# Kernel optimization log

Measured on AMD Instinct MI355X. Metric: run time of the kernel, lower is better.

## Reference

```python
import jax, jax.numpy as jnp
import numpy as np

WS = 7       # window_size
SHIFT = 3    # shift_size
HEADS = 3
EPS = 1e-5


def _rel_index():
    # (2, N) coords of a WS x WS window, then pairwise relative offsets -> flat table index
    coords = np.stack(np.meshgrid(np.arange(WS), np.arange(WS), indexing='ij')).reshape(2, -1)
    rel = (coords[:, :, None] - coords[:, None, :]).transpose(1, 2, 0) + (WS - 1)  # (N,N,2)
    return jnp.asarray(rel[..., 0] * (2 * WS - 1) + rel[..., 1])  # (N,N) int


def _layernorm(x, g, b):
    mu = jnp.mean(x, axis=-1, keepdims=True)
    var = jnp.mean(jnp.square(x - mu), axis=-1, keepdims=True)
    return (x - mu) * jax.lax.rsqrt(var + EPS) * g + b


def setup_inputs() -> dict:
    key = jax.random.key(0)
    ks = jax.random.split(key, 6)
    C, HID = 96, 384
    s = 0.02
    return {
        'x': jax.random.normal(ks[0], (8, C, 224, 224), jnp.float32),
        'norm1_g': jnp.ones((C,), jnp.float32),
        'norm1_b': jnp.zeros((C,), jnp.float32),
        'qkv_w': jax.random.normal(ks[1], (C, 3 * C), jnp.float32) * s,
        'qkv_b': jnp.zeros((3 * C,), jnp.float32),
        'proj_w': jax.random.normal(ks[2], (C, C), jnp.float32) * s,
        'proj_b': jnp.zeros((C,), jnp.float32),
        'rel_bias_table': jax.random.normal(ks[3], ((2 * WS - 1) ** 2, HEADS), jnp.float32) * s,
        'norm2_g': jnp.ones((C,), jnp.float32),
        'norm2_b': jnp.zeros((C,), jnp.float32),
        'fc1_w': jax.random.normal(ks[4], (C, HID), jnp.float32) * s,
        'fc1_b': jnp.zeros((HID,), jnp.float32),
        'fc2_w': jax.random.normal(ks[5], (HID, C), jnp.float32) * s,
        'fc2_b': jnp.zeros((C,), jnp.float32),
    }


def reference(x, norm1_g, norm1_b, qkv_w, qkv_b, proj_w, proj_b,
              rel_bias_table, norm2_g, norm2_b, fc1_w, fc1_b, fc2_w, fc2_b):
    B, C, H, W = x.shape
    N = WS * WS
    dh = C // HEADS

    # norm1 over channels (tokens = flattened spatial)
    xt = x.reshape(B, C, H * W).transpose(0, 2, 1)          # (B, L, C)
    xn = _layernorm(xt, norm1_g, norm1_b)
    xs = xn.transpose(0, 2, 1).reshape(B, C, H, W)
    # H, W divisible by WS -> pad is a no-op; cyclic shift
    xs = jnp.roll(xs, (-SHIFT, -SHIFT), axis=(2, 3))

    # window partition -> (B*nW, N, C)
    xw = xs.reshape(B, C, H // WS, WS, W // WS, WS)
    xw = xw.transpose(0, 2, 4, 3, 5, 1).reshape(-1, N, C)

    # window attention with relative position bias (no shift mask, per source)
    Bw = xw.shape[0]
    qkv = (xw @ qkv_w + qkv_b).reshape(Bw, N, 3, HEADS, dh).transpose(2, 0, 3, 1, 4)
    q, k, v = qkv[0], qkv[1], qkv[2]                        # (Bw, h, N, dh)
    attn = jnp.einsum('bhnd,bhmd->bhnm', q, k) * (dh ** -0.5)
    bias = rel_bias_table[_rel_index().reshape(-1)].reshape(N, N, HEADS).transpose(2, 0, 1)
    attn = jax.nn.softmax(attn + bias, axis=-1)
    out = jnp.einsum('bhnm,bhmd->bhnd', attn, v).transpose(0, 2, 1, 3).reshape(Bw, N, C)
    out = out @ proj_w + proj_b

    # window reverse + unshift
    xr = out.reshape(B, H // WS, W // WS, WS, WS, C)
    xr = xr.transpose(0, 5, 1, 3, 2, 4).reshape(B, C, H, W)
    xr = jnp.roll(xr, (SHIFT, SHIFT), axis=(2, 3))

    x = x + xr                                              # residual 1

    # MLP branch with norm2 (exact GELU, matching torch nn.GELU default)
    xt = x.reshape(B, C, H * W).transpose(0, 2, 1)
    xn = _layernorm(xt, norm2_g, norm2_b)
    h = jax.nn.gelu(xn @ fc1_w + fc1_b, approximate=False)
    h = h @ fc2_w + fc2_b
    return x + h.transpose(0, 2, 1).reshape(B, C, H, W)
```

## Files before the change

### kernel.cpp

```cpp
#include <hip/hip_runtime.h>
#include <hip/hip_bf16.h>
#include <math.h>

#define WSZ 7
#define NTOK 49
#define CH 96
#define HIMG 224
#define WIMG 224
#define HWIMG (224*224)
#define SHIFT_ 3
#define HID 384

typedef __attribute__((ext_vector_type(8))) short bf16x8;
typedef __attribute__((ext_vector_type(4))) float f32x4;
typedef unsigned int u32;
typedef unsigned short u16;

__device__ __forceinline__ u32 pk2(float a, float b) {
    u16 ua = __builtin_bit_cast(u16, __float2bfloat16(a));
    u16 ub = __builtin_bit_cast(u16, __float2bfloat16(b));
    return (u32)ua | ((u32)ub << 16);
}
__device__ __forceinline__ float bflo(u32 u) { return __builtin_bit_cast(float, u << 16); }

union FragU { u32 w[4]; bf16x8 v; };

__device__ __forceinline__ bf16x8 regroup(u32 t0w0, u32 t0w1, u32 t1w0, u32 t1w1, int lane) {
    int sl0 = (lane & 15) + ((lane & 16) << 1);
    int sl1 = sl0 + 16;
    u32 x0 = (u32)__shfl((int)t0w0, sl0);
    u32 y0 = (u32)__shfl((int)t1w0, sl0);
    u32 x1 = (u32)__shfl((int)t0w1, sl0);
    u32 y1 = (u32)__shfl((int)t1w1, sl0);
    u32 x2 = (u32)__shfl((int)t0w0, sl1);
    u32 y2 = (u32)__shfl((int)t1w0, sl1);
    u32 x3 = (u32)__shfl((int)t0w1, sl1);
    u32 y3 = (u32)__shfl((int)t1w1, sl1);
    bool lo = lane < 32;
    FragU f;
    f.w[0] = lo ? x0 : y0;
    f.w[1] = lo ? x1 : y1;
    f.w[2] = lo ? x2 : y2;
    f.w[3] = lo ? x3 : y3;
    return f.v;
}

__device__ __forceinline__ float gelu_f(float x) {
    float x2 = x * x;
    float s  = x * (0.7978845608028654f + 0.03567740813636141f * x2);
    float e  = __expf(2.0f * s);
    float th = 1.0f - 2.0f / (e + 1.0f);
    return 0.5f * x * (1.0f + th);
}

__global__ __launch_bounds__(256) void prep_kernel(
    const float* __restrict__ w1, const float* __restrict__ w2,
    const float* __restrict__ pw, const float* __restrict__ qw,
    __hip_bfloat16* __restrict__ ws, int n)
{
    int i = blockIdx.x * 256 + threadIdx.x;
    if (i >= n) return;
    float val = 0.f;
    if (i < 81920) {
        int ch = i / 20480, r = i - ch * 20480;
        int half = r / 10240;
        int rr = r - half * 10240;
        if (rr < 9984) {
            int row = rr / 104, col = rr - row * 104;
            if (col < 96)
                val = (half == 0) ? w1[col * HID + ch * 96 + row]
                                  : w2[(size_t)(ch * 96 + col) * CH + row];
        }
    } else if (i < 92160) {
        int r = i - 81920;
        if (r < 9984) {
            int row = r / 104, col = r - row * 104;
            if (col < 96) val = pw[col * CH + row];
        }
    } else {
        int j = i - 92160;
        int hh = j / 9984, rr = j - hh * 9984;
        int dp = rr / 104, c = rr - dp * 104;
        if (c < 96) {
            int colW = (dp < 32) ? (hh * 32 + dp)
                     : (dp < 64) ? (96 + hh * 32 + dp - 32)
                                 : (192 + hh * 32 + dp - 64);
            val = qw[c * 288 + colW];
        }
    }
    ws[i] = __float2bfloat16(val);
}

__global__ __launch_bounds__(256) void attn2_kernel(
    const float* __restrict__ x,
    const float* __restrict__ g1, const float* __restrict__ b1,
    const __hip_bfloat16* __restrict__ wsW,
    const float* __restrict__ qkv_b, const float* __restrict__ pb,
    const float* __restrict__ btab,
    __hip_bfloat16* __restrict__ projout)
{
    const int tid  = threadIdx.x;
    const int lane = tid & 63;
    const int wv   = tid >> 6;
    const int l15  = lane & 15;
    const int g    = lane >> 4;
    const int bi   = blockIdx.x;
    const int b    = bi >> 8;
    const int wh   = (bi >> 3) & 31;
    const int ww0  = (bi & 7) * 4;
    const int ww   = ww0 + wv;

    __shared__ float btabL[507];
    __shared__ __align__(16) char uniA[43008];

    __hip_bfloat16 (*xsb)[7][32] = (__hip_bfloat16(*)[7][32])uniA;
    __hip_bfloat16 (*vT)[72] = (__hip_bfloat16(*)[72])(uniA + wv * 4608);
    u32* prS = (u32*)(uniA + wv * 4608);

    for (int idx = tid; idx < 507; idx += 256) btabL[idx] = btab[idx];

    const int colBase = ww0 * 7 + 3;
    const int cA  = colBase & ~3;
    const int cb4 = cA >> 2;
    const int a0  = colBase & 3;
    #pragma unroll
    for (int k = 0; k < 21; ++k) {
        int idx = tid + 256 * k;
        int c = idx / 56, rem = idx - c * 56;
        int r = rem >> 3, cf = rem & 7;
        int gr = wh * 7 + 3 + r; if (gr >= HIMG) gr -= HIMG;
        int g4 = cb4 + cf; if (g4 >= 56) g4 -= 56;
        float4 v = *(const float4*)(x + ((size_t)(b * CH + c) * HIMG + gr) * WIMG + g4 * 4);
        uint2 pk;
        pk.x = pk2(v.x, v.y);
        pk.y = pk2(v.z, v.w);
        *(uint2*)&xsb[c][r][cf * 4] = pk;
    }
    __syncthreads();

    bf16x8 xB[4][3];
    #pragma unroll
    for (int it = 0; it < 4; ++it) {
        int i = it * 16 + l15;
        bool real = i < NTOK;
        int yi = i / 7, xi = i - yi * 7;
        int sc = a0 + wv * 7 + xi;
        float raw[24];
        float s0 = 0.f, s1 = 0.f;
        #pragma unroll
        for (int ks = 0; ks < 3; ++ks)
            #pragma unroll
            for (int t = 0; t < 8; ++t) {
                int c = ks * 32 + g * 8 + t;
                float v = real ? __bfloat162float(xsb[c][yi][sc]) : 0.f;
                raw[ks * 8 + t] = v; s0 += v; s1 += v * v;
            }
        s0 += __shfl_xor(s0, 16); s0 += __shfl_xor(s0, 32);
        s1 += __shfl_xor(s1, 16); s1 += __shfl_xor(s1, 32);
        float mu = s0 * (1.0f / CH);
        float rstd = rsqrtf(s1 * (1.0f / CH) - mu * mu + 1e-5f);
        #pragma unroll
        for (int ks = 0; ks < 3; ++ks)
            #pragma unroll
            for (int t = 0; t < 8; ++t) {
                int c = ks * 32 + g * 8 + t;
                float xv = real ? ((raw[ks * 8 + t] - mu) * rstd * g1[c] + b1[c]) : 0.f;
                xB[it][ks][t] = (short)__builtin_bit_cast(u16, __float2bfloat16(xv));
            }
    }
    __syncthreads();

    const float scale = 0.17677669529663687f;
    bf16x8 aoB[3][4];

    for (int h = 0; h < 3; ++h) {
        const __hip_bfloat16* qkvTg = wsW + 92160 + h * 9984;

        float qb[2][4], kb[2][4], vb[2][4];
        #pragma unroll
        for (int dt = 0; dt < 2; ++dt)
            #pragma unroll
            for (int r = 0; r < 4; ++r) {
                int d = h * 32 + dt * 16 + g * 4 + r;
                qb[dt][r] = qkv_b[d];
                kb[dt][r] = qkv_b[96 + d];
                vb[dt][r] = qkv_b[192 + d];
            }

        u32 Qpk[2][4][2];
        #pragma unroll
        for (int dt = 0; dt < 2; ++dt) {
            const __hip_bfloat16* wr = qkvTg + (dt * 16 + l15) * 104 + g * 8;
            bf16x8 a0f = *(const bf16x8*)(wr);
            bf16x8 a1f = *(const bf16x8*)(wr + 32);
            bf16x8 a2f = *(const bf16x8*)(wr + 64);
            #pragma unroll
            for (int it = 0; it < 4; ++it) {
                f32x4 c4 = {0.f, 0.f, 0.f, 0.f};
                c4 = __builtin_amdgcn_mfma_f32_16x16x32_bf16(a0f, xB[it][0], c4, 0, 0, 0);
                c4 = __builtin_amdgcn_mfma_f32_16x16x32_bf16(a1f, xB[it][1], c4, 0, 0, 0);
                c4 = __builtin_amdgcn_mfma_f32_16x16x32_bf16(a2f, xB[it][2], c4, 0, 0, 0);
                Qpk[dt][it][0] = pk2(c4[0] + qb[dt][0], c4[1] + qb[dt][1]);
                Qpk[dt][it][1] = pk2(c4[2] + qb[dt][2], c4[3] + qb[dt][3]);
            }
        }
        bf16x8 QB[4];
        #pragma unroll
        for (int it = 0; it < 4; ++it)
            QB[it] = regroup(Qpk[0][it][0], Qpk[0][it][1], Qpk[1][it][0], Qpk[1][it][1], lane);

        u32 Kpk[2][4][2];
        #pragma unroll
        for (int dt = 0; dt < 2; ++dt) {
            const __hip_bfloat16* wr = qkvTg + (32 + dt * 16 + l15) * 104 + g * 8;
            bf16x8 a0f = *(const bf16x8*)(wr);
            bf16x8 a1f = *(const bf16x8*)(wr + 32);
            bf16x8 a2f = *(const bf16x8*)(wr + 64);
            #pragma unroll
            for (int it = 0; it < 4; ++it) {
                f32x4 c4 = {0.f, 0.f, 0.f, 0.f};
                c4 = __builtin_amdgcn_mfma_f32_16x16x32_bf16(a0f, xB[it][0], c4, 0, 0, 0);
                c4 = __builtin_amdgcn_mfma_f32_16x16x32_bf16(a1f, xB[it][1], c4, 0, 0, 0);
                c4 = __builtin_amdgcn_mfma_f32_16x16x32_bf16(a2f, xB[it][2], c4, 0, 0, 0);
                Kpk[dt][it][0] = pk2(c4[0] + kb[dt][0], c4[1] + kb[dt][1]);
                Kpk[dt][it][1] = pk2(c4[2] + kb[dt][2], c4[3] + kb[dt][3]);
            }
        }
        bf16x8 KA[4];
        #pragma unroll
        for (int it = 0; it < 4; ++it)
            KA[it] = regroup(Kpk[0][it][0], Kpk[0][it][1], Kpk[1][it][0], Kpk[1][it][1], lane);

        #pragma unroll
        for (int dt = 0; dt < 2; ++dt) {
            const __hip_bfloat16* wr = qkvTg + (64 + dt * 16 + l15) * 104 + g * 8;
            bf16x8 a0f = *(const bf16x8*)(wr);
            bf16x8 a1f = *(const bf16x8*)(wr + 32);
            bf16x8 a2f = *(const bf16x8*)(wr + 64);
            #pragma unroll
            for (int it = 0; it < 4; ++it) {
                f32x4 c4 = {0.f, 0.f, 0.f, 0.f};
                c4 = __builtin_amdgcn_mfma_f32_16x16x32_bf16(a0f, xB[it][0], c4, 0, 0, 0);
                c4 = __builtin_amdgcn_mfma_f32_16x16x32_bf16(a1f, xB[it][1], c4, 0, 0, 0);
                c4 = __builtin_amdgcn_mfma_f32_16x16x32_bf16(a2f, xB[it][2], c4, 0, 0, 0);
                #pragma unroll
                for (int r = 0; r < 4; ++r)
                    vT[dt * 16 + g * 4 + r][it * 16 + l15] = __float2bfloat16(c4[r] + vb[dt][r]);
            }
        }
        bf16x8 VBf[2][2];
        #pragma unroll
        for (int dt = 0; dt < 2; ++dt)
            #pragma unroll
            for (int ks = 0; ks < 2; ++ks)
                VBf[dt][ks] = *(const bf16x8*)&vT[dt * 16 + l15][ks * 32 + g * 8];

        #pragma unroll
        for (int it = 0; it < 4; ++it) {
            f32x4 SC[4];
            #pragma unroll
            for (int jt = 0; jt < 4; ++jt) {
                f32x4 z = {0.f, 0.f, 0.f, 0.f};
                SC[jt] = __builtin_amdgcn_mfma_f32_16x16x32_bf16(KA[jt], QB[it], z, 0, 0, 0);
            }
            int i = it * 16 + l15;
            int yi = i / 7, xi = i - yi * 7;
            float p[16];
            float m = -1e30f;
            #pragma unroll
            for (int jt = 0; jt < 4; ++jt)
                #pragma unroll
                for (int r = 0; r < 4; ++r) {
                    int j = jt * 16 + g * 4 + r;
                    int yj = j / 7, xj = j - yj * 7;
                    int rel = (yi - yj + 6) * 13 + (xi - xj + 6);
                    rel = rel < 0 ? 0 : (rel > 168 ? 168 : rel);
                    float s = (j < NTOK) ? (SC[jt][r] * scale + btabL[rel * 3 + h]) : -1e30f;
                    p[jt * 4 + r] = s;
                    m = fmaxf(m, s);
                }
            m = fmaxf(m, __shfl_xor(m, 16));
            m = fmaxf(m, __shfl_xor(m, 32));
            float sum = 0.f;
            #pragma unroll
            for (int q = 0; q < 16; ++q) { float e = __expf(p[q] - m); p[q] = e; sum += e; }
            sum += __shfl_xor(sum, 16);
            sum += __shfl_xor(sum, 32);
            float inv = 1.f / sum;
            u32 Ppk[4][2];
            #pragma unroll
            for (int jt = 0; jt < 4; ++jt) {
                Ppk[jt][0] = pk2(p[jt * 4 + 0] * inv, p[jt * 4 + 1] * inv);
                Ppk[jt][1] = pk2(p[jt * 4 + 2] * inv, p[jt * 4 + 3] * inv);
            }
            bf16x8 PA0 = regroup(Ppk[0][0], Ppk[0][1], Ppk[1][0], Ppk[1][1], lane);
            bf16x8 PA1 = regroup(Ppk[2][0], Ppk[2][1], Ppk[3][0], Ppk[3][1], lane);
            u32 opk[2][2];
            #pragma unroll
            for (int dt = 0; dt < 2; ++dt) {
                f32x4 o = {0.f, 0.f, 0.f, 0.f};
                o = __builtin_amdgcn_mfma_f32_16x16x32_bf16(PA0, VBf[dt][0], o, 0, 0, 0);
                o = __builtin_amdgcn_mfma_f32_16x16x32_bf16(PA1, VBf[dt][1], o, 0, 0, 0);
                opk[dt][0] = pk2(o[0], o[1]);
                opk[dt][1] = pk2(o[2], o[3]);
            }
            aoB[h][it] = regroup(opk[0][0], opk[0][1], opk[1][0], opk[1][1], lane);
        }
    }

    const __hip_bfloat16* pwTg = wsW + 81920;
    for (int it = 0; it < 4; ++it) {
        #pragma unroll
        for (int mt = 0; mt < 6; ++mt) {
            const __hip_bfloat16* wr = pwTg + (mt * 16 + l15) * 104 + g * 8;
            f32x4 cp = {0.f, 0.f, 0.f, 0.f};
            #pragma unroll
            for (int ks = 0; ks < 3; ++ks) {
                bf16x8 af = *(const bf16x8*)(wr + ks * 32);
                cp = __builtin_amdgcn_mfma_f32_16x16x32_bf16(af, aoB[ks][it], cp, 0, 0, 0);
            }
            float v0 = cp[0] + pb[mt * 16 + g * 4 + 0];
            float v1 = cp[1] + pb[mt * 16 + g * 4 + 1];
            float v2 = cp[2] + pb[mt * 16 + g * 4 + 2];
            float v3 = cp[3] + pb[mt * 16 + g * 4 + 3];
            prS[l15 * 52 + mt * 8 + g * 2 + 0] = pk2(v0, v1);
            prS[l15 * 52 + mt * 8 + g * 2 + 1] = pk2(v2, v3);
        }
        #pragma unroll
        for (int s = 0; s < 3; ++s) {
            int chunk = lane + 64 * s;
            int row = chunk / 12, q = chunk - row * 12;
            int tok = it * 16 + row;
            if (tok < NTOK) {
                int yi = tok / 7, xi = tok - yi * 7;
                int hh = wh * 7 + yi + SHIFT_; if (hh >= HIMG) hh -= HIMG;
                int wp = ww * 7 + xi + SHIFT_; if (wp >= WIMG) wp -= WIMG;
                float4 val = *(const float4*)((const char*)prS + row * 208 + q * 16);
                *(float4*)(projout + ((size_t)b * HWIMG + hh * WIMG + wp) * 96 + q * 8) = val;
            }
        }
    }
}

__global__ __launch_bounds__(512, 4) void mlp2_kernel(
    const float* __restrict__ x, const __hip_bfloat16* __restrict__ projout,
    const float* __restrict__ g2, const float* __restrict__ b2,
    const float* __restrict__ bb1, const float* __restrict__ bb2,
    const __hip_bfloat16* __restrict__ wsW,
    float* __restrict__ out)
{
    const int tid = threadIdx.x;
    const int lane = tid & 63, wv = tid >> 6;
    const int l15 = lane & 15, g = lane >> 4;
    const int b = blockIdx.x / 392;
    const int hw0 = (blockIdx.x % 392) * 128;
    const int tok = wv * 16 + l15;

    __shared__ __align__(16) char SB[26624];
    __shared__ float bb1S[HID];

    __hip_bfloat16 (*xnS)[104]  = (__hip_bfloat16(*)[104])SB;
    __hip_bfloat16 (*wT)[104]   = (__hip_bfloat16(*)[104])SB;
    __hip_bfloat16 (*obuf)[104] = (__hip_bfloat16(*)[104])SB;

    #pragma unroll
    for (int s = 0; s < 3; ++s) {
        int chunk = tid + 512 * s;
        int row = chunk / 12, q = chunk - row * 12;
        *(float4*)&xnS[row][q * 8] =
            *(const float4*)(projout + ((size_t)b * HWIMG + hw0 + row) * 96 + q * 8);
    }
    for (int idx = tid; idx < HID; idx += 512) bb1S[idx] = bb1[idx];
    __syncthreads();

    float xr[24];
    float s0 = 0.f, s1 = 0.f;
    bf16x8 pf[3];
    #pragma unroll
    for (int ks = 0; ks < 3; ++ks)
        pf[ks] = *(const bf16x8*)&xnS[tok][ks * 32 + g * 8];
    const float* xb = x + (size_t)(b * CH) * HWIMG + hw0 + tok;
    #pragma unroll
    for (int ks = 0; ks < 3; ++ks)
        #pragma unroll
        for (int j = 0; j < 8; ++j) {
            int c = ks * 32 + g * 8 + j;
            float xv = xb[(size_t)c * HWIMG];
            float v = xv + bflo((u32)(u16)pf[ks][j]);
            xr[ks * 8 + j] = v; s0 += v; s1 += v * v;
        }
    s0 += __shfl_xor(s0, 16); s0 += __shfl_xor(s0, 32);
    s1 += __shfl_xor(s1, 16); s1 += __shfl_xor(s1, 32);
    float mu = s0 * (1.0f / CH);
    float rstd = rsqrtf(s1 * (1.0f / CH) - mu * mu + 1e-5f);

    bf16x8 xbf[3];
    #pragma unroll
    for (int ks = 0; ks < 3; ++ks) {
        float nv[8];
        #pragma unroll
        for (int j = 0; j < 8; ++j) {
            int c = ks * 32 + g * 8 + j;
            nv[j] = (xr[ks * 8 + j] - mu) * rstd * g2[c] + b2[c];
        }
        FragU f;
        f.w[0] = pk2(nv[0], nv[1]); f.w[1] = pk2(nv[2], nv[3]);
        f.w[2] = pk2(nv[4], nv[5]); f.w[3] = pk2(nv[6], nv[7]);
        xbf[ks] = f.v;
    }
    __syncthreads();

    f32x4 acc[6];
    #pragma unroll
    for (int mt = 0; mt < 6; ++mt) {
        #pragma unroll
        for (int r = 0; r < 4; ++r) acc[mt][r] = bb2[mt * 16 + g * 4 + r];
    }

    for (int ch = 0; ch < 4; ++ch) {
        {
            const float4* src = (const float4*)wsW + (size_t)ch * 2560;
            #pragma unroll
            for (int i = tid; i < 1280; i += 512) ((float4*)SB)[i] = src[i];
        }
        __syncthreads();

        u32 hpk[6][2];
        #pragma unroll
        for (int mt = 0; mt < 6; ++mt) {
            f32x4 f = {0.f, 0.f, 0.f, 0.f};
            #pragma unroll
            for (int ks = 0; ks < 3; ++ks) {
                bf16x8 af = *(const bf16x8*)&wT[mt * 16 + l15][ks * 32 + g * 8];
                f = __builtin_amdgcn_mfma_f32_16x16x32_bf16(af, xbf[ks], f, 0, 0, 0);
            }
            float gl[4];
            #pragma unroll
            for (int r = 0; r < 4; ++r) {
                float a = f[r] + bb1S[ch * 96 + mt * 16 + g * 4 + r];
                gl[r] = gelu_f(a);
            }
            hpk[mt][0] = pk2(gl[0], gl[1]);
            hpk[mt][1] = pk2(gl[2], gl[3]);
        }
        __syncthreads();

        {
            const float4* src = (const float4*)wsW + (size_t)ch * 2560 + 1280;
            #pragma unroll
            for (int i = tid; i < 1280; i += 512) ((float4*)SB)[i] = src[i];
        }
        __syncthreads();

        bf16x8 hf[3];
        hf[0] = regroup(hpk[0][0], hpk[0][1], hpk[1][0], hpk[1][1], lane);
        hf[1] = regroup(hpk[2][0], hpk[2][1], hpk[3][0], hpk[3][1], lane);
        hf[2] = regroup(hpk[4][0], hpk[4][1], hpk[5][0], hpk[5][1], lane);

        #pragma unroll
        for (int mt = 0; mt < 6; ++mt) {
            #pragma unroll
            for (int ks = 0; ks < 3; ++ks) {
                bf16x8 af = *(const bf16x8*)&wT[mt * 16 + l15][ks * 32 + g * 8];
                acc[mt] = __builtin_amdgcn_mfma_f32_16x16x32_bf16(af, hf[ks], acc[mt], 0, 0, 0);
            }
        }
        __syncthreads();
    }

    #pragma unroll
    for (int mt = 0; mt < 6; ++mt)
        #pragma unroll
        for (int r = 0; r < 4; ++r)
            obuf[tok][mt * 16 + g * 4 + r] = __float2bfloat16(acc[mt][r]);
    __syncthreads();
    #pragma unroll
    for (int ks = 0; ks < 3; ++ks) {
        bf16x8 ov = *(const bf16x8*)&obuf[tok][ks * 32 + g * 8];
        #pragma unroll
        for (int j = 0; j < 8; ++j) {
            int c = ks * 32 + g * 8 + j;
            out[(size_t)(b * CH + c) * HWIMG + hw0 + tok] =
                xr[ks * 8 + j] + bflo((u32)(u16)ov[j]);
        }
    }
}

__global__ __launch_bounds__(256) void attn_mfma_kernel(
    const float* __restrict__ x,
    const float* __restrict__ g1, const float* __restrict__ b1,
    const float* __restrict__ qkv_w, const float* __restrict__ qkv_b,
    const float* __restrict__ btab,
    float* __restrict__ ao)
{
    const int tid  = threadIdx.x;
    const int lane = tid & 63;
    const int wv   = tid >> 6;
    const int l15  = lane & 15;
    const int g    = lane >> 4;
    const int wid  = blockIdx.x * 4 + wv;
    const int b    = wid >> 10;
    const int wh   = (wid >> 5) & 31;
    const int ww   = wid & 31;

    __shared__ __align__(16) __hip_bfloat16 wT[96][104];
    __shared__ float btabL[507];
    __shared__ __align__(16) __hip_bfloat16 vT[4][32][72];
    __shared__ __align__(16) __hip_bfloat16 Ob[4][64][36];

    int to_h = 0, to_w = 0;
    if (lane < NTOK) {
        int yl = lane / 7, xl = lane - yl * 7;
        to_h = wh * 7 + yl + SHIFT_; if (to_h >= HIMG) to_h -= HIMG;
        to_w = ww * 7 + xl + SHIFT_; if (to_w >= WIMG) to_w -= WIMG;
    }

    bf16x8 xB[4][3];
    #pragma unroll
    for (int it = 0; it < 4; ++it) {
        int i = it * 16 + l15;
        bool real = i < NTOK;
        int yi = i / 7, xi = i - yi * 7;
        int hh = wh * 7 + yi + SHIFT_; if (hh >= HIMG) hh -= HIMG;
        int wp = ww * 7 + xi + SHIFT_; if (wp >= WIMG) wp -= WIMG;
        float raw[24];
        float s0 = 0.f, s1 = 0.f;
        #pragma unroll
        for (int ks = 0; ks < 3; ++ks)
            #pragma unroll
            for (int t = 0; t < 8; ++t) {
                int c = ks * 32 + g * 8 + t;
                float v = real ? x[((size_t)(b * CH + c) * HIMG + hh) * WIMG + wp] : 0.f;
                raw[ks * 8 + t] = v; s0 += v; s1 += v * v;
            }
        s0 += __shfl_xor(s0, 16); s0 += __shfl_xor(s0, 32);
        s1 += __shfl_xor(s1, 16); s1 += __shfl_xor(s1, 32);
        float mu = s0 * (1.0f / CH);
        float rstd = rsqrtf(s1 * (1.0f / CH) - mu * mu + 1e-5f);
        #pragma unroll
        for (int ks = 0; ks < 3; ++ks)
            #pragma unroll
            for (int t = 0; t < 8; ++t) {
                int c = ks * 32 + g * 8 + t;
                float xv = real ? ((raw[ks * 8 + t] - mu) * rstd * g1[c] + b1[c]) : 0.f;
                xB[it][ks][t] = (short)__builtin_bit_cast(u16, __float2bfloat16(xv));
            }
    }

    const float scale = 0.17677669529663687f;

    for (int h = 0; h < 3; ++h) {
        __syncthreads();
        for (int idx = tid; idx < 96 * 96; idx += 256) {
            int c = idx / 96, dp = idx - c * 96;
            int col = (dp < 32) ? (h * 32 + dp) : (dp < 64) ? (96 + h * 32 + dp - 32)
                                                            : (192 + h * 32 + dp - 64);
            wT[dp][c] = __float2bfloat16(qkv_w[c * 288 + col]);
        }
        if (h == 0)
            for (int idx = tid; idx < 507; idx += 256) btabL[idx] = btab[idx];
        __syncthreads();

        float qb[2][4], kb[2][4], vb[2][4];
        #pragma unroll
        for (int dt = 0; dt < 2; ++dt)
            #pragma unroll
            for (int r = 0; r < 4; ++r) {
                int d = h * 32 + dt * 16 + g * 4 + r;
                qb[dt][r] = qkv_b[d];
                kb[dt][r] = qkv_b[96 + d];
                vb[dt][r] = qkv_b[192 + d];
            }

        u32 Qpk[2][4][2];
        #pragma unroll
        for (int dt = 0; dt < 2; ++dt) {
            bf16x8 a0 = *(const bf16x8*)&wT[dt * 16 + l15][0 * 32 + g * 8];
            bf16x8 a1 = *(const bf16x8*)&wT[dt * 16 + l15][1 * 32 + g * 8];
            bf16x8 a2 = *(const bf16x8*)&wT[dt * 16 + l15][2 * 32 + g * 8];
            #pragma unroll
            for (int it = 0; it < 4; ++it) {
                f32x4 c4 = {0.f, 0.f, 0.f, 0.f};
                c4 = __builtin_amdgcn_mfma_f32_16x16x32_bf16(a0, xB[it][0], c4, 0, 0, 0);
                c4 = __builtin_amdgcn_mfma_f32_16x16x32_bf16(a1, xB[it][1], c4, 0, 0, 0);
                c4 = __builtin_amdgcn_mfma_f32_16x16x32_bf16(a2, xB[it][2], c4, 0, 0, 0);
                Qpk[dt][it][0] = pk2(c4[0] + qb[dt][0], c4[1] + qb[dt][1]);
                Qpk[dt][it][1] = pk2(c4[2] + qb[dt][2], c4[3] + qb[dt][3]);
            }
        }
        bf16x8 QB[4];
        #pragma unroll
        for (int it = 0; it < 4; ++it)
            QB[it] = regroup(Qpk[0][it][0], Qpk[0][it][1], Qpk[1][it][0], Qpk[1][it][1], lane);

        u32 Kpk[2][4][2];
        #pragma unroll
        for (int dt = 0; dt < 2; ++dt) {
            bf16x8 a0 = *(const bf16x8*)&wT[32 + dt * 16 + l15][0 * 32 + g * 8];
            bf16x8 a1 = *(const bf16x8*)&wT[32 + dt * 16 + l15][1 * 32 + g * 8];
            bf16x8 a2 = *(const bf16x8*)&wT[32 + dt * 16 + l15][2 * 32 + g * 8];
            #pragma unroll
            for (int it = 0; it < 4; ++it) {
                f32x4 c4 = {0.f, 0.f, 0.f, 0.f};
                c4 = __builtin_amdgcn_mfma_f32_16x16x32_bf16(a0, xB[it][0], c4, 0, 0, 0);
                c4 = __builtin_amdgcn_mfma_f32_16x16x32_bf16(a1, xB[it][1], c4, 0, 0, 0);
                c4 = __builtin_amdgcn_mfma_f32_16x16x32_bf16(a2, xB[it][2], c4, 0, 0, 0);
                Kpk[dt][it][0] = pk2(c4[0] + kb[dt][0], c4[1] + kb[dt][1]);
                Kpk[dt][it][1] = pk2(c4[2] + kb[dt][2], c4[3] + kb[dt][3]);
            }
        }
        bf16x8 KA[4];
        #pragma unroll
        for (int it = 0; it < 4; ++it)
            KA[it] = regroup(Kpk[0][it][0], Kpk[0][it][1], Kpk[1][it][0], Kpk[1][it][1], lane);

        #pragma unroll
        for (int dt = 0; dt < 2; ++dt) {
            bf16x8 a0 = *(const bf16x8*)&wT[64 + dt * 16 + l15][0 * 32 + g * 8];
            bf16x8 a1 = *(const bf16x8*)&wT[64 + dt * 16 + l15][1 * 32 + g * 8];
            bf16x8 a2 = *(const bf16x8*)&wT[64 + dt * 16 + l15][2 * 32 + g * 8];
            #pragma unroll
            for (int it = 0; it < 4; ++it) {
                f32x4 c4 = {0.f, 0.f, 0.f, 0.f};
                c4 = __builtin_amdgcn_mfma_f32_16x16x32_bf16(a0, xB[it][0], c4, 0, 0, 0);
                c4 = __builtin_amdgcn_mfma_f32_16x16x32_bf16(a1, xB[it][1], c4, 0, 0, 0);
                c4 = __builtin_amdgcn_mfma_f32_16x16x32_bf16(a2, xB[it][2], c4, 0, 0, 0);
                #pragma unroll
                for (int r = 0; r < 4; ++r)
                    vT[wv][dt * 16 + g * 4 + r][it * 16 + l15] = __float2bfloat16(c4[r] + vb[dt][r]);
            }
        }
        bf16x8 VBf[2][2];
        #pragma unroll
        for (int dt = 0; dt < 2; ++dt)
            #pragma unroll
            for (int ks = 0; ks < 2; ++ks)
                VBf[dt][ks] = *(const bf16x8*)&vT[wv][dt * 16 + l15][ks * 32 + g * 8];

        #pragma unroll
        for (int it = 0; it < 4; ++it) {
            f32x4 SC[4];
            #pragma unroll
            for (int jt = 0; jt < 4; ++jt) {
                f32x4 z = {0.f, 0.f, 0.f, 0.f};
                SC[jt] = __builtin_amdgcn_mfma_f32_16x16x32_bf16(KA[jt], QB[it], z, 0, 0, 0);
            }
            int i = it * 16 + l15;
            int yi = i / 7, xi = i - yi * 7;
            float p[16];
            float m = -1e30f;
            #pragma unroll
            for (int jt = 0; jt < 4; ++jt)
                #pragma unroll
                for (int r = 0; r < 4; ++r) {
                    int j = jt * 16 + g * 4 + r;
                    int yj = j / 7, xj = j - yj * 7;
                    int rel = (yi - yj + 6) * 13 + (xi - xj + 6);
                    rel = rel < 0 ? 0 : (rel > 168 ? 168 : rel);
                    float s = (j < NTOK) ? (SC[jt][r] * scale + btabL[rel * 3 + h]) : -1e30f;
                    p[jt * 4 + r] = s;
                    m = fmaxf(m, s);
                }
            m = fmaxf(m, __shfl_xor(m, 16));
            m = fmaxf(m, __shfl_xor(m, 32));
            float sum = 0.f;
            #pragma unroll
            for (int q = 0; q < 16; ++q) { float e = __expf(p[q] - m); p[q] = e; sum += e; }
            sum += __shfl_xor(sum, 16);
            sum += __shfl_xor(sum, 32);
            float inv = 1.f / sum;
            u32 Ppk[4][2];
            #pragma unroll
            for (int jt = 0; jt < 4; ++jt) {
                Ppk[jt][0] = pk2(p[jt * 4 + 0] * inv, p[jt * 4 + 1] * inv);
                Ppk[jt][1] = pk2(p[jt * 4 + 2] * inv, p[jt * 4 + 3] * inv);
            }
            bf16x8 PA0 = regroup(Ppk[0][0], Ppk[0][1], Ppk[1][0], Ppk[1][1], lane);
            bf16x8 PA1 = regroup(Ppk[2][0], Ppk[2][1], Ppk[3][0], Ppk[3][1], lane);
            #pragma unroll
            for (int dt = 0; dt < 2; ++dt) {
                f32x4 o = {0.f, 0.f, 0.f, 0.f};
                o = __builtin_amdgcn_mfma_f32_16x16x32_bf16(PA0, VBf[dt][0], o, 0, 0, 0);
                o = __builtin_amdgcn_mfma_f32_16x16x32_bf16(PA1, VBf[dt][1], o, 0, 0, 0);
                #pragma unroll
                for (int r = 0; r < 4; ++r)
                    Ob[wv][it * 16 + g * 4 + r][dt * 16 + l15] = __float2bfloat16(o[r]);
            }
        }

        if (lane < NTOK) {
            #pragma unroll 8
            for (int ch = 0; ch < 32; ++ch)
                ao[((size_t)(b * CH + h * 32 + ch) * HIMG + to_h) * WIMG + to_w] =
                    __bfloat162float(Ob[wv][lane][ch]);
        }
    }
}

__global__ __launch_bounds__(512, 4) void fuse2_kernel(
    const float* __restrict__ x, const float* ao,
    const float* __restrict__ pw, const float* __restrict__ pb,
    const float* __restrict__ g2, const float* __restrict__ b2,
    const float* __restrict__ w1, const float* __restrict__ bb1,
    const float* __restrict__ w2, const float* __restrict__ bb2,
    const __hip_bfloat16* __restrict__ wsW, int useWs,
    float* out)
{
    const int tid = threadIdx.x;
    const int lane = tid & 63, wv = tid >> 6;
    const int l15 = lane & 15, g = lane >> 4;
    const int b = blockIdx.x / 392;
    const int hw0 = (blockIdx.x % 392) * 128;
    const int m0 = wv * 16;
    const int t = tid & 127;
    const int c0 = tid >> 7;

    __shared__ __align__(16) char WREG[46592];
    __shared__ __align__(16) __hip_bfloat16 xnS[128][104];
    __shared__ float part0[4][128], part1[4][128];
    __shared__ float muS[128], rsS[128];
    __shared__ float bb1S[HID];

    __hip_bfloat16 (*pwT)[104]   = (__hip_bfloat16(*)[104])WREG;
    __hip_bfloat16 (*projS)[104] = (__hip_bfloat16(*)[104])(WREG + 19968);
    __hip_bfloat16 (*w1T)[104]   = (__hip_bfloat16(*)[104])WREG;
    __hip_bfloat16 (*w2T)[104]   = (__hip_bfloat16(*)[104])(WREG + 20480);
    __hip_bfloat16 (*obuf)[104]  = (__hip_bfloat16(*)[104])WREG;

    float xreg[24];

    for (int idx = tid, k = 0; idx < 96 * 128; idx += 512, ++k) {
        int c = idx >> 7, tt = idx & 127;
        size_t gi = (size_t)(b * CH + c) * HWIMG + hw0 + tt;
        xreg[k] = x[gi];
        xnS[tt][c] = __float2bfloat16(ao[gi]);
    }
    if (useWs) {
        const float4* src = (const float4*)wsW + 10240;
        float4* dst = (float4*)WREG;
        for (int i = tid; i < 1280; i += 512) dst[i] = src[i];
    } else {
        for (int idx = tid; idx < 96 * 96; idx += 512) {
            int c = idx / 96, oc = idx - c * 96;
            pwT[oc][c] = __float2bfloat16(pw[c * 96 + oc]);
        }
    }
    for (int idx = tid; idx < HID; idx += 512) bb1S[idx] = bb1[idx];
    __syncthreads();

    {
        bf16x8 bfr[3];
        #pragma unroll
        for (int ks = 0; ks < 3; ++ks)
            bfr[ks] = *(const bf16x8*)&xnS[m0 + l15][ks * 32 + g * 8];
        #pragma unroll
        for (int mt = 0; mt < 6; ++mt) {
            f32x4 cp = {0.f, 0.f, 0.f, 0.f};
            #pragma unroll
            for (int ks = 0; ks < 3; ++ks) {
                bf16x8 af = *(const bf16x8*)&pwT[mt * 16 + l15][ks * 32 + g * 8];
                cp = __builtin_amdgcn_mfma_f32_16x16x32_bf16(af, bfr[ks], cp, 0, 0, 0);
            }
            #pragma unroll
            for (int r = 0; r < 4; ++r) {
                int oc = mt * 16 + g * 4 + r;
                projS[m0 + l15][oc] = __float2bfloat16(cp[r] + pb[oc]);
            }
        }
    }
    __syncthreads();

    {
        float s0 = 0.f, s1 = 0.f;
        #pragma unroll
        for (int k = 0; k < 24; ++k) {
            int c = c0 + 4 * k;
            float v = xreg[k] + __bfloat162float(projS[t][c]);
            xreg[k] = v; s0 += v; s1 += v * v;
        }
        part0[c0][t] = s0; part1[c0][t] = s1;
    }
    __syncthreads();
    if (tid < 128) {
        float s0 = part0[0][tid] + part0[1][tid] + part0[2][tid] + part0[3][tid];
        float s1 = part1[0][tid] + part1[1][tid] + part1[2][tid] + part1[3][tid];
        float m = s0 * (1.0f / CH);
        muS[tid] = m;
        rsS[tid] = rsqrtf(s1 * (1.0f / CH) - m * m + 1e-5f);
    }
    __syncthreads();
    #pragma unroll
    for (int k = 0; k < 24; ++k) {
        int c = c0 + 4 * k;
        xnS[t][c] = __float2bfloat16((xreg[k] - muS[t]) * rsS[t] * g2[c] + b2[c]);
    }
    __syncthreads();

    bf16x8 xbf[3];
    #pragma unroll
    for (int ks = 0; ks < 3; ++ks)
        xbf[ks] = *(const bf16x8*)&xnS[m0 + l15][ks * 32 + g * 8];

    f32x4 acc[6];
    #pragma unroll
    for (int mt = 0; mt < 6; ++mt)
        #pragma unroll
        for (int r = 0; r < 4; ++r)
            acc[mt][r] = bb2[mt * 16 + g * 4 + r];

    for (int ch = 0; ch < 4; ++ch) {
        if (useWs) {
            const float4* src = (const float4*)wsW + (size_t)ch * 2560;
            float4* dst = (float4*)WREG;
            #pragma unroll
            for (int i = tid; i < 2560; i += 512) dst[i] = src[i];
        } else {
            for (int idx = tid; idx < 2 * 96 * 96; idx += 512) {
                if (idx < 9216) {
                    int kk = idx / 96, n = idx - kk * 96;
                    w1T[n][kk] = __float2bfloat16(w1[kk * HID + ch * 96 + n]);
                } else {
                    int j = idx - 9216;
                    int kk = j / 96, n = j - kk * 96;
                    w2T[n][kk] = __float2bfloat16(w2[(size_t)(ch * 96 + kk) * CH + n]);
                }
            }
        }
        __syncthreads();

        u32 hpk[6][2];
        #pragma unroll
        for (int mt = 0; mt < 6; ++mt) {
            f32x4 f = {0.f, 0.f, 0.f, 0.f};
            #pragma unroll
            for (int ks = 0; ks < 3; ++ks) {
                bf16x8 af = *(const bf16x8*)&w1T[mt * 16 + l15][ks * 32 + g * 8];
                f = __builtin_amdgcn_mfma_f32_16x16x32_bf16(af, xbf[ks], f, 0, 0, 0);
            }
            float gl[4];
            #pragma unroll
            for (int r = 0; r < 4; ++r) {
                float a = f[r] + bb1S[ch * 96 + mt * 16 + g * 4 + r];
                gl[r] = gelu_f(a);
            }
            hpk[mt][0] = pk2(gl[0], gl[1]);
            hpk[mt][1] = pk2(gl[2], gl[3]);
        }
        bf16x8 hf[3];
        hf[0] = regroup(hpk[0][0], hpk[0][1], hpk[1][0], hpk[1][1], lane);
        hf[1] = regroup(hpk[2][0], hpk[2][1], hpk[3][0], hpk[3][1], lane);
        hf[2] = regroup(hpk[4][0], hpk[4][1], hpk[5][0], hpk[5][1], lane);

        #pragma unroll
        for (int mt = 0; mt < 6; ++mt)
            #pragma unroll
            for (int ks = 0; ks < 3; ++ks) {
                bf16x8 af = *(const bf16x8*)&w2T[mt * 16 + l15][ks * 32 + g * 8];
                acc[mt] = __builtin_amdgcn_mfma_f32_16x16x32_bf16(af, hf[ks], acc[mt], 0, 0, 0);
            }
        __syncthreads();
    }

    #pragma unroll
    for (int mt = 0; mt < 6; ++mt)
        #pragma unroll
        for (int r = 0; r < 4; ++r)
            obuf[m0 + l15][mt * 16 + g * 4 + r] = __float2bfloat16(acc[mt][r]);
    __syncthreads();
    #pragma unroll
    for (int k = 0; k < 24; ++k) {
        int c = c0 + 4 * k;
        out[(size_t)(b * CH + c) * HWIMG + hw0 + t] = xreg[k] + __bfloat162float(obuf[t][c]);
    }
}

extern "C" void kernel_launch(void* const* d_in, const int* in_sizes, int n_in,
                              void* d_out, int out_size, void* d_ws, size_t ws_size,
                              hipStream_t stream) {
    const float* x    = (const float*)d_in[0];
    const float* n1g  = (const float*)d_in[1];
    const float* n1b  = (const float*)d_in[2];
    const float* qkvw = (const float*)d_in[3];
    const float* qkvb = (const float*)d_in[4];
    const float* pw   = (const float*)d_in[5];
    const float* pbv  = (const float*)d_in[6];
    const float* bt   = (const float*)d_in[7];
    const float* n2g  = (const float*)d_in[8];
    const float* n2b  = (const float*)d_in[9];
    const float* f1w  = (const float*)d_in[10];
    const float* f1b  = (const float*)d_in[11];
    const float* f2w  = (const float*)d_in[12];
    const float* f2b  = (const float*)d_in[13];
    float* out = (float*)d_out;

    const size_t FULL_NEED = 262144ull + 77070336ull;
    if (ws_size >= FULL_NEED) {
        __hip_bfloat16* wsW = (__hip_bfloat16*)d_ws;
        __hip_bfloat16* projout = (__hip_bfloat16*)((char*)d_ws + 262144);
        prep_kernel<<<477, 256, 0, stream>>>(f1w, f2w, pw, qkvw, wsW, 122112);
        attn2_kernel<<<2048, 256, 0, stream>>>(x, n1g, n1b, wsW, qkvb, pbv, bt, projout);
        mlp2_kernel<<<3136, 512, 0, stream>>>(x, projout, n2g, n2b, f1b, f2b, wsW, out);
    } else {
        int useWs = (ws_size >= 184320) ? 1 : 0;
        if (useWs)
            prep_kernel<<<360, 256, 0, stream>>>(f1w, f2w, pw, qkvw, (__hip_bfloat16*)d_ws, 92160);
        attn_mfma_kernel<<<2048, 256, 0, stream>>>(x, n1g, n1b, qkvw, qkvb, bt, out);
        fuse2_kernel<<<3136, 512, 0, stream>>>(x, out, pw, pbv, n2g, n2b, f1w, f1b, f2w, f2b,
                                               (const __hip_bfloat16*)d_ws, useWs, out);
    }
}
```

Before: 458.2 us.

## Double-buffer MLP weight staging via registers and coalesce output stores

The MLP kernel now prefetches the next weight chunk from global memory into registers while the current chunk's MFMAs run, writing it into a second LDS buffer. This removes the serialized load-then-sync before each GEMM stage. The epilogue stages the fp32 residual sum in LDS so global writes are coalesced along the spatial dimension, and the output is no longer rounded to bf16. GELU is rewritten with fewer operations using a hardware reciprocal. LDS per block grows to about 50KB, which may cut occupancy below the requested 4 blocks.

```diff
diff --git a/kernel.cpp b/kernel.cpp
--- a/kernel.cpp
+++ b/kernel.cpp
@@ -47,10 +47,10 @@
 
 __device__ __forceinline__ float gelu_f(float x) {
     float x2 = x * x;
-    float s  = x * (0.7978845608028654f + 0.03567740813636141f * x2);
-    float e  = __expf(2.0f * s);
-    float th = 1.0f - 2.0f / (e + 1.0f);
-    return 0.5f * x * (1.0f + th);
+    float t  = x * (1.5957691216057308f + 0.07135481283587191f * x2);
+    float e  = __expf(t);
+    float r  = __builtin_amdgcn_rcpf(e + 1.0f);
+    return x - x * r;
 }
 
 __global__ __launch_bounds__(256) void prep_kernel(
@@ -342,6 +342,11 @@
     }
 }
 
+#define LDSTG(p0, p1, p2, s) { const float4* _s = wsrc + (s) * 1280; \
+    p0 = _s[tid]; p1 = _s[tid + 512]; if (tid < 256) p2 = _s[tid + 1024]; }
+#define WRSTG(p0, p1, p2, off) { float4* _d = (float4*)(SB + (off)); \
+    _d[tid] = p0; _d[tid + 512] = p1; if (tid < 256) _d[tid + 1024] = p2; }
+
 __global__ __launch_bounds__(512, 4) void mlp2_kernel(
     const float* __restrict__ x, const __hip_bfloat16* __restrict__ projout,
     const float* __restrict__ g2, const float* __restrict__ b2,
@@ -356,12 +361,18 @@
     const int hw0 = (blockIdx.x % 392) * 128;
     const int tok = wv * 16 + l15;
 
-    __shared__ __align__(16) char SB[26624];
+    __shared__ __align__(16) char SB[50688];
     __shared__ float bb1S[HID];
 
-    __hip_bfloat16 (*xnS)[104]  = (__hip_bfloat16(*)[104])SB;
-    __hip_bfloat16 (*wT)[104]   = (__hip_bfloat16(*)[104])SB;
-    __hip_bfloat16 (*obuf)[104] = (__hip_bfloat16(*)[104])SB;
+    __hip_bfloat16 (*xnS)[104] = (__hip_bfloat16(*)[104])SB;
+    __hip_bfloat16 (*wT0)[104] = (__hip_bfloat16(*)[104])SB;
+    __hip_bfloat16 (*wT1)[104] = (__hip_bfloat16(*)[104])(SB + 20480);
+    float* ob = (float*)SB;
+
+    const float4* wsrc = (const float4*)wsW;
+    float4 ra0, ra1, ra2, rb0, rb1, rb2;
+
+    LDSTG(ra0, ra1, ra2, 0);
 
     #pragma unroll
     for (int s = 0; s < 3; ++s) {
@@ -410,6 +421,10 @@
     }
     __syncthreads();
 
+    WRSTG(ra0, ra1, ra2, 0);
+    LDSTG(rb0, rb1, rb2, 1);
+    __syncthreads();
+
     f32x4 acc[6];
     #pragma unroll
     for (int mt = 0; mt < 6; ++mt) {
@@ -417,21 +432,15 @@
         for (int r = 0; r < 4; ++r) acc[mt][r] = bb2[mt * 16 + g * 4 + r];
     }
 
+    #pragma unroll
     for (int ch = 0; ch < 4; ++ch) {
-        {
-            const float4* src = (const float4*)wsW + (size_t)ch * 2560;
-            #pragma unroll
-            for (int i = tid; i < 1280; i += 512) ((float4*)SB)[i] = src[i];
-        }
-        __syncthreads();
-
         u32 hpk[6][2];
         #pragma unroll
         for (int mt = 0; mt < 6; ++mt) {
             f32x4 f = {0.f, 0.f, 0.f, 0.f};
             #pragma unroll
             for (int ks = 0; ks < 3; ++ks) {
-                bf16x8 af = *(const bf16x8*)&wT[mt * 16 + l15][ks * 32 + g * 8];
+                bf16x8 af = *(const bf16x8*)&wT0[mt * 16 + l15][ks * 32 + g * 8];
                 f = __builtin_amdgcn_mfma_f32_16x16x32_bf16(af, xbf[ks], f, 0, 0, 0);
             }
             float gl[4];
@@ -443,46 +452,44 @@
             hpk[mt][0] = pk2(gl[0], gl[1]);
             hpk[mt][1] = pk2(gl[2], gl[3]);
         }
+        WRSTG(rb0, rb1, rb2, 20480);
         __syncthreads();
-
-        {
-            const float4* src = (const float4*)wsW + (size_t)ch * 2560 + 1280;
-            #pragma unroll
-            for (int i = tid; i < 1280; i += 512) ((float4*)SB)[i] = src[i];
-        }
-        __syncthreads();
+        if (ch < 3) LDSTG(ra0, ra1, ra2, 2 * ch + 2);
 
         bf16x8 hf[3];
         hf[0] = regroup(hpk[0][0], hpk[0][1], hpk[1][0], hpk[1][1], lane);
         hf[1] = regroup(hpk[2][0], hpk[2][1], hpk[3][0], hpk[3][1], lane);
         hf[2] = regroup(hpk[4][0], hpk[4][1], hpk[5][0], hpk[5][1], lane);
-
         #pragma unroll
         for (int mt = 0; mt < 6; ++mt) {
             #pragma unroll
             for (int ks = 0; ks < 3; ++ks) {
-                bf16x8 af = *(const bf16x8*)&wT[mt * 16 + l15][ks * 32 + g * 8];
+                bf16x8 af = *(const bf16x8*)&wT1[mt * 16 + l15][ks * 32 + g * 8];
                 acc[mt] = __builtin_amdgcn_mfma_f32_16x16x32_bf16(af, hf[ks], acc[mt], 0, 0, 0);
             }
         }
+        if (ch < 3) WRSTG(ra0, ra1, ra2, 0);
         __syncthreads();
-    }
-
+        if (ch < 3) LDSTG(rb0, rb1, rb2, 2 * ch + 3);
+    }
+
+    #pragma unroll
+    for (int ks = 0; ks < 3; ++ks)
+        #pragma unroll
+        for (int j = 0; j < 8; ++j)
+            ob[tok * 99 + ks * 32 + g * 8 + j] = xr[ks * 8 + j];
+    __syncthreads();
     #pragma unroll
     for (int mt = 0; mt < 6; ++mt)
         #pragma unroll
         for (int r = 0; r < 4; ++r)
-            obuf[tok][mt * 16 + g * 4 + r] = __float2bfloat16(acc[mt][r]);
-    __syncthreads();
-    #pragma unroll
-    for (int ks = 0; ks < 3; ++ks) {
-        bf16x8 ov = *(const bf16x8*)&obuf[tok][ks * 32 + g * 8];
-        #pragma unroll
-        for (int j = 0; j < 8; ++j) {
-            int c = ks * 32 + g * 8 + j;
-            out[(size_t)(b * CH + c) * HWIMG + hw0 + tok] =
-                xr[ks * 8 + j] + bflo((u32)(u16)ov[j]);
-        }
+            ob[tok * 99 + mt * 16 + g * 4 + r] += acc[mt][r];
+    __syncthreads();
+    #pragma unroll
+    for (int k = 0; k < 24; ++k) {
+        int idx = tid + 512 * k;
+        int c = idx >> 7, t = idx & 127;
+        out[(size_t)(b * CH + c) * HWIMG + hw0 + t] = ob[t * 99 + c];
     }
 }
 
```

New measurement: 405.5 us. 11.5% less time.
